# Kernel optimization log

Measured on AMD Instinct MI355X. Metric: run time of the kernel, lower is better.

## Reference

```python
import jax, jax.numpy as jnp
import numpy as np

H = 8   # n_heads
C = 2   # top-k scale factor: topk = int(C * log(L))


def setup_inputs() -> dict:
    key = jax.random.key(0)
    k1, k2, k3 = jax.random.split(key, 3)
    B, L, D = 16, 512, 4096  # L == D // H required by the original broadcasting
    Q = jax.random.normal(k1, (B, L, D), dtype=jnp.float32)
    K = jax.random.normal(k2, (B, L, D), dtype=jnp.float32)
    V = jax.random.normal(k3, (B, L, D), dtype=jnp.float32)
    return {"Q": Q, "K": K, "V": V}


def _autocorrelation(Q, K, V):
    B, L, D = Q.shape
    d = D // H
    # [B,L,D] -> [B,H,L,d]
    q = Q.reshape(B, L, H, d).transpose(0, 2, 1, 3)
    k = K.reshape(B, L, H, d).transpose(0, 2, 1, 3)
    v = V.reshape(B, L, H, d).transpose(0, 2, 1, 3)
    # FFT-based autocorrelation along the time axis (per head, per channel)
    qf = jnp.fft.fft(q, axis=2)
    kf = jnp.fft.fft(k, axis=2)
    corr = jnp.fft.ifft(qf * jnp.conj(kf), axis=2).real  # [B,H,L,d]
    topk = int(C * np.log(L))  # static: 12 for L=512
    # top-k delays per (batch, head, channel): move L to last axis
    w, idx = jax.lax.top_k(corr.transpose(0, 1, 3, 2), topk)  # [B,H,d,topk]
    w = jax.nn.softmax(w, axis=-1)
    pos = jnp.arange(L)[:, None]  # [L,1]
    out = jnp.zeros_like(v)       # [B,H,L,d]
    # small fixed loop over topk ~ O(log L) delays: gather + scale + accumulate
    for i in range(topk):
        g = jnp.minimum(idx[:, :, None, :, i] + pos, L - 1)        # [B,H,L,d]
        out = out + w[:, :, None, :, i] * jnp.take_along_axis(v, g, axis=2)
    return out.transpose(0, 2, 1, 3).reshape(B, L, D)


def reference(Q, K, V):
    return _autocorrelation(Q, K, V)
```

## Files before the change

kernel.cpp:

```cpp
#include <hip/hip_runtime.h>

#define L_LEN 512
#define D_DIM 4096
#define H_NUM 8
#define B_NUM 16
#define TOPK  12


#define LOADQK(QV, KV, QWOFF, TOFF) do {                                      \
    _Pragma("unroll")                                                         \
    for (int x = 0; x < 4; ++x) {                                             \
      const float4 v = *(const float4*)(qc + (QWOFF) + 4 * x);                \
      QV[4*x+0] = v.x; QV[4*x+1] = v.y; QV[4*x+2] = v.z; QV[4*x+3] = v.w;     \
    }                                                                         \
    _Pragma("unroll")                                                         \
    for (int x = 0; x < 4; ++x) {                                             \
      const float4 v = *(const float4*)(qc + (QWOFF) + 20 + 4 * x);           \
      QV[16+4*x+0] = v.x; QV[16+4*x+1] = v.y;                                 \
      QV[16+4*x+2] = v.z; QV[16+4*x+3] = v.w;                                 \
    }                                                                         \
    _Pragma("unroll")                                                         \
    for (int x = 0; x < 4; ++x) {                                             \
      const float4 v = *(const float4*)(kc + (TOFF) + 4 * x);                 \
      KV[4*x+0] = v.x; KV[4*x+1] = v.y; KV[4*x+2] = v.z; KV[4*x+3] = v.w;     \
    }                                                                         \
  } while (0)

#define MACBLK(QV, KV) do {                                                   \
    _Pragma("unroll")                                                         \
    for (int tt = 0; tt < 16; ++tt)                                           \
      _Pragma("unroll")                                                       \
      for (int ii = 0; ii < 16; ++ii)                                         \
        acc[ii] = fmaf(QV[ii + tt], KV[tt], acc[ii]);                         \
  } while (0)

__global__ __launch_bounds__(256, 2) void corr_topk_kernel(
    const float* __restrict__ Q, const float* __restrict__ K,
    float* __restrict__ ws_w, int* __restrict__ ws_i)
{
  __shared__ float qs[8][1312];
  __shared__ float ks[8][544];

  const int tid = threadIdx.x;
  const int bid = blockIdx.x;
  const int work = (bid & 7) * 1024 + (bid >> 3);
  const int bh   = work >> 6;
  const int cblk = work & 63;
  const int c0   = cblk * 8;

  const size_t base = (size_t)(bh >> 3) * (size_t)(L_LEN * D_DIM)
                    + (size_t)(bh & 7) * 512 + c0;

  #pragma unroll
  for (int rep = 0; rep < 4; ++rep) {
    const int idx  = rep * 256 + tid;
    const int t    = idx >> 1;
    const int half = idx & 1;
    const float4 qv = *(const float4*)(Q + base + (size_t)t * D_DIM + half * 4);
    const float4 kv = *(const float4*)(K + base + (size_t)t * D_DIM + half * 4);
    const int w  = t + ((t >> 4) << 2);
    const int cb = half * 4;
    const float qa[4] = {qv.x, qv.y, qv.z, qv.w};
    const float ka[4] = {kv.x, kv.y, kv.z, kv.w};
    #pragma unroll
    for (int j = 0; j < 4; ++j) {
      qs[cb + j][w]       = qa[j];
      qs[cb + j][w + 640] = qa[j];
      ks[cb + j][t]       = ka[j];
    }
  }
  __syncthreads();

  const int wave = tid >> 6;
  const int lane = tid & 63;
  const int ch   = wave * 2 + (lane >> 5);
  const int m    = lane & 31;

  const float* __restrict__ qc = qs[ch];
  const float* __restrict__ kc = ks[ch];

  float acc[16];
  #pragma unroll
  for (int i = 0; i < 16; ++i) acc[i] = 0.f;

  int qw = 20 * m;
  float qvA[32], kvA[16], qvB[32], kvB[16];
  LOADQK(qvA, kvA, qw, 0);
  #pragma unroll 1
  for (int t0 = 0; t0 < 512; t0 += 32) {
    LOADQK(qvB, kvB, qw + 20, t0 + 16);
    MACBLK(qvA, kvA);
    LOADQK(qvA, kvA, qw + 40, t0 + 32);
    MACBLK(qvB, kvB);
    qw += 40;
  }

  const int tau0 = m * 16;
  float bv[TOPK]; int bi[TOPK];
  #pragma unroll
  for (int s = 0; s < TOPK; ++s) {
    float lv = acc[0]; int li = 0;
    #pragma unroll
    for (int i = 1; i < 16; ++i) if (acc[i] > lv) { lv = acc[i]; li = i; }
    int gi = tau0 + li;
    #pragma unroll
    for (int off = 16; off >= 1; off >>= 1) {
      const float ov = __shfl_xor(lv, off, 32);
      const int   oi = __shfl_xor(gi, off, 32);
      if (ov > lv || (ov == lv && oi < gi)) { lv = ov; gi = oi; }
    }
    bv[s] = lv; bi[s] = gi;
    const int slot = gi - tau0;
    #pragma unroll
    for (int i = 0; i < 16; ++i) acc[i] = (slot == i) ? -3.4e38f : acc[i];
  }

  float e[TOPK]; float sum = 0.f;
  #pragma unroll
  for (int s = 0; s < TOPK; ++s) { e[s] = expf(bv[s] - bv[0]); sum += e[s]; }
  const float inv = 1.f / sum;

  if (m == 0) {
    const int g = (bh * 512 + c0 + ch) * TOPK;
    #pragma unroll
    for (int s = 0; s < TOPK; ++s) { ws_w[g + s] = e[s] * inv; ws_i[g + s] = bi[s]; }
  }
}

__global__ __launch_bounds__(512, 4) void gather_kernel(
    const float* __restrict__ V, const float* __restrict__ ws_w,
    const int* __restrict__ ws_i, float* __restrict__ out)
{
  __shared__ float vs[512][32];

  const int tid = threadIdx.x;
  const int bid = blockIdx.x;
  const int work = (bid & 7) * 256 + (bid >> 3);
  const int b  = work >> 7;
  const int dg = work & 127;
  const int d0 = dg * 32;
  const int h  = d0 >> 9;
  const int c0 = d0 & 511;

  const size_t vcol = (size_t)b * (size_t)(L_LEN * D_DIM) + d0;

  const int cl   = tid & 31;
  const int tsub = tid >> 5;

  float4 stga, stgb;
  const int e0 = tid, e1 = 512 + tid;
  const int ra0 = e0 >> 3, qa0 = (e0 & 7) * 4;
  const int rb0 = e1 >> 3, qb0 = (e1 & 7) * 4;

  stga = *(const float4*)(V + vcol + (size_t)(3 * 128 + ra0) * D_DIM + qa0);
  stgb = *(const float4*)(V + vcol + (size_t)(3 * 128 + rb0) * D_DIM + qb0);

  const int g = ((b * 8 + h) * 512 + c0 + cl) * TOPK;
  float w[TOPK]; int r0[TOPK];
  #pragma unroll
  for (int s = 0; s < TOPK; ++s) { w[s] = ws_w[g + s]; r0[s] = ws_i[g + s]; }

  const size_t ob = vcol + cl;

  #pragma unroll 1
  for (int ph = 3; ph >= 0; --ph) {
    *(float4*)(&vs[ph * 128 + ra0][qa0]) = stga;
    *(float4*)(&vs[ph * 128 + rb0][qb0]) = stgb;
    if (ph > 0) {
      stga = *(const float4*)(V + vcol + (size_t)((ph - 1) * 128 + ra0) * D_DIM + qa0);
      stgb = *(const float4*)(V + vcol + (size_t)((ph - 1) * 128 + rb0) * D_DIM + qb0);
    }
    asm volatile("s_waitcnt lgkmcnt(0)" ::: "memory");
    __builtin_amdgcn_s_barrier();
    asm volatile("" ::: "memory");

    #pragma unroll
    for (int k8 = 0; k8 < 8; ++k8) {
      const int t = ph * 128 + (k8 << 4) + tsub;
      float a = 0.f;
      #pragma unroll
      for (int s = 0; s < TOPK; ++s) {
        int r = r0[s] + t;
        r = r > (L_LEN - 1) ? (L_LEN - 1) : r;
        a = fmaf(w[s], vs[r][cl], a);
      }
      out[ob + (size_t)t * D_DIM] = a;
    }
  }
}

extern "C" void kernel_launch(void* const* d_in, const int* in_sizes, int n_in,
                              void* d_out, int out_size, void* d_ws, size_t ws_size,
                              hipStream_t stream)
{
  const float* Q = (const float*)d_in[0];
  const float* K = (const float*)d_in[1];
  const float* V = (const float*)d_in[2];
  float* out = (float*)d_out;

  float* ws_w = (float*)d_ws;
  int*   ws_i = (int*)((char*)d_ws + (size_t)B_NUM * H_NUM * 512 * TOPK * sizeof(float));

  corr_topk_kernel<<<dim3(B_NUM * H_NUM * 64), dim3(256), 0, stream>>>(Q, K, ws_w, ws_i);
  gather_kernel<<<dim3(B_NUM * H_NUM * 16), dim3(512), 0, stream>>>(V, ws_w, ws_i, out);
}
```

Baseline: 808.3 us.

## Map one channel per wave with 8 lags per lane and XOR-swizzled LDS

The correlation kernel now uses 512 threads per block. Each wave owns one channel and each lane computes 8 lags instead of 16, which cuts accumulator and register pressure and raises the occupancy target. Q is stored in LDS with an XOR swizzle in place of padding, and a rolling 32-entry register buffer replaces the double-buffered Q/K register arrays. The top-k reduction now shuffles across the full 64-lane wave. In exchange, each lane has fewer FMAs per LDS load, which lowers arithmetic intensity per LDS access.

```diff
diff --git a/kernel.cpp b/kernel.cpp
--- a/kernel.cpp
+++ b/kernel.cpp
@@ -7,112 +7,121 @@
 #define TOPK  12
 
 
-#define LOADQK(QV, KV, QWOFF, TOFF) do {                                      \
-    _Pragma("unroll")                                                         \
-    for (int x = 0; x < 4; ++x) {                                             \
-      const float4 v = *(const float4*)(qc + (QWOFF) + 4 * x);                \
-      QV[4*x+0] = v.x; QV[4*x+1] = v.y; QV[4*x+2] = v.z; QV[4*x+3] = v.w;     \
-    }                                                                         \
-    _Pragma("unroll")                                                         \
-    for (int x = 0; x < 4; ++x) {                                             \
-      const float4 v = *(const float4*)(qc + (QWOFF) + 20 + 4 * x);           \
-      QV[16+4*x+0] = v.x; QV[16+4*x+1] = v.y;                                 \
-      QV[16+4*x+2] = v.z; QV[16+4*x+3] = v.w;                                 \
-    }                                                                         \
-    _Pragma("unroll")                                                         \
-    for (int x = 0; x < 4; ++x) {                                             \
-      const float4 v = *(const float4*)(kc + (TOFF) + 4 * x);                 \
-      KV[4*x+0] = v.x; KV[4*x+1] = v.y; KV[4*x+2] = v.z; KV[4*x+3] = v.w;     \
-    }                                                                         \
+#define QADDR(W) (qc + (((((W) >> 2) ^ (((W) >> 5) & 1)) << 2) | ((W) & 3)))
+
+#define ITER(P, I) do {                                                      \
+    const int t0 = (I) * 16;                                                 \
+    const float4 r0_ = *(const float4*)QADDR(tau0 + t0 + 32);                \
+    const float4 r1_ = *(const float4*)QADDR(tau0 + t0 + 36);                \
+    const float4 r2_ = *(const float4*)QADDR(tau0 + t0 + 40);                \
+    const float4 r3_ = *(const float4*)QADDR(tau0 + t0 + 44);                \
+    const float4 ka_ = *(const float4*)(kc + t0);                            \
+    const float4 kb_ = *(const float4*)(kc + t0 + 4);                        \
+    {                                                                        \
+      const float kk[8] = {ka_.x,ka_.y,ka_.z,ka_.w, kb_.x,kb_.y,kb_.z,kb_.w};\
+      _Pragma("unroll")                                                      \
+      for (int tt = 0; tt < 8; ++tt)                                         \
+        _Pragma("unroll")                                                    \
+        for (int ii = 0; ii < 8; ++ii)                                       \
+          acc[ii] = fmaf(qb[((P) + ii + tt) & 31], kk[tt], acc[ii]);         \
+    }                                                                        \
+    const float4 kc_ = *(const float4*)(kc + t0 + 8);                        \
+    const float4 kd_ = *(const float4*)(kc + t0 + 12);                       \
+    {                                                                        \
+      const float kk[8] = {kc_.x,kc_.y,kc_.z,kc_.w, kd_.x,kd_.y,kd_.z,kd_.w};\
+      _Pragma("unroll")                                                      \
+      for (int tt = 0; tt < 8; ++tt)                                         \
+        _Pragma("unroll")                                                    \
+        for (int ii = 0; ii < 8; ++ii)                                       \
+          acc[ii] = fmaf(qb[((P) + 8 + ii + tt) & 31], kk[tt], acc[ii]);     \
+    }                                                                        \
+    qb[(P)+ 0]=r0_.x; qb[(P)+ 1]=r0_.y; qb[(P)+ 2]=r0_.z; qb[(P)+ 3]=r0_.w;  \
+    qb[(P)+ 4]=r1_.x; qb[(P)+ 5]=r1_.y; qb[(P)+ 6]=r1_.z; qb[(P)+ 7]=r1_.w;  \
+    qb[(P)+ 8]=r2_.x; qb[(P)+ 9]=r2_.y; qb[(P)+10]=r2_.z; qb[(P)+11]=r2_.w;  \
+    qb[(P)+12]=r3_.x; qb[(P)+13]=r3_.y; qb[(P)+14]=r3_.z; qb[(P)+15]=r3_.w;  \
   } while (0)
 
-#define MACBLK(QV, KV) do {                                                   \
-    _Pragma("unroll")                                                         \
-    for (int tt = 0; tt < 16; ++tt)                                           \
-      _Pragma("unroll")                                                       \
-      for (int ii = 0; ii < 16; ++ii)                                         \
-        acc[ii] = fmaf(QV[ii + tt], KV[tt], acc[ii]);                         \
-  } while (0)
-
-__global__ __launch_bounds__(256, 2) void corr_topk_kernel(
+__global__ __launch_bounds__(512, 4) void corr_topk_kernel(
     const float* __restrict__ Q, const float* __restrict__ K,
     float* __restrict__ ws_w, int* __restrict__ ws_i)
 {
-  __shared__ float qs[8][1312];
-  __shared__ float ks[8][544];
+  __shared__ float qs[8][1056];
+  __shared__ float ks[8][512];
 
   const int tid = threadIdx.x;
   const int bid = blockIdx.x;
   const int work = (bid & 7) * 1024 + (bid >> 3);
   const int bh   = work >> 6;
-  const int cblk = work & 63;
-  const int c0   = cblk * 8;
+  const int c0   = (work & 63) * 8;
 
   const size_t base = (size_t)(bh >> 3) * (size_t)(L_LEN * D_DIM)
                     + (size_t)(bh & 7) * 512 + c0;
 
   #pragma unroll
-  for (int rep = 0; rep < 4; ++rep) {
-    const int idx  = rep * 256 + tid;
+  for (int rep = 0; rep < 2; ++rep) {
+    const int idx  = rep * 512 + tid;
     const int t    = idx >> 1;
     const int half = idx & 1;
     const float4 qv = *(const float4*)(Q + base + (size_t)t * D_DIM + half * 4);
     const float4 kv = *(const float4*)(K + base + (size_t)t * D_DIM + half * 4);
-    const int w  = t + ((t >> 4) << 2);
+    const int pw = ((((t >> 2) ^ ((t >> 5) & 1)) << 2) | (t & 3));
     const int cb = half * 4;
     const float qa[4] = {qv.x, qv.y, qv.z, qv.w};
     const float ka[4] = {kv.x, kv.y, kv.z, kv.w};
     #pragma unroll
     for (int j = 0; j < 4; ++j) {
-      qs[cb + j][w]       = qa[j];
-      qs[cb + j][w + 640] = qa[j];
-      ks[cb + j][t]       = ka[j];
+      qs[cb + j][pw]       = qa[j];
+      qs[cb + j][pw + 512] = qa[j];
+      ks[cb + j][t]        = ka[j];
+    }
+    if (t < 32) {
+      #pragma unroll
+      for (int j = 0; j < 4; ++j) qs[cb + j][pw + 1024] = qa[j];
     }
   }
   __syncthreads();
 
-  const int wave = tid >> 6;
+  const int wv   = __builtin_amdgcn_readfirstlane(tid >> 6);
   const int lane = tid & 63;
-  const int ch   = wave * 2 + (lane >> 5);
-  const int m    = lane & 31;
-
-  const float* __restrict__ qc = qs[ch];
-  const float* __restrict__ kc = ks[ch];
-
-  float acc[16];
-  #pragma unroll
-  for (int i = 0; i < 16; ++i) acc[i] = 0.f;
-
-  int qw = 20 * m;
-  float qvA[32], kvA[16], qvB[32], kvB[16];
-  LOADQK(qvA, kvA, qw, 0);
+  const int tau0 = lane * 8;
+
+  const float* __restrict__ qc = qs[wv];
+  const float* __restrict__ kc = ks[wv];
+
+  float acc[8];
+  #pragma unroll
+  for (int i = 0; i < 8; ++i) acc[i] = 0.f;
+
+  float qb[32];
+  #pragma unroll
+  for (int x = 0; x < 8; ++x) {
+    const float4 v = *(const float4*)QADDR(tau0 + 4 * x);
+    qb[4*x] = v.x; qb[4*x+1] = v.y; qb[4*x+2] = v.z; qb[4*x+3] = v.w;
+  }
+
   #pragma unroll 1
-  for (int t0 = 0; t0 < 512; t0 += 32) {
-    LOADQK(qvB, kvB, qw + 20, t0 + 16);
-    MACBLK(qvA, kvA);
-    LOADQK(qvA, kvA, qw + 40, t0 + 32);
-    MACBLK(qvB, kvB);
-    qw += 40;
-  }
-
-  const int tau0 = m * 16;
+  for (int i = 0; i < 32; i += 2) {
+    ITER(0, i);
+    ITER(16, i + 1);
+  }
+
   float bv[TOPK]; int bi[TOPK];
   #pragma unroll
   for (int s = 0; s < TOPK; ++s) {
     float lv = acc[0]; int li = 0;
     #pragma unroll
-    for (int i = 1; i < 16; ++i) if (acc[i] > lv) { lv = acc[i]; li = i; }
+    for (int i = 1; i < 8; ++i) if (acc[i] > lv) { lv = acc[i]; li = i; }
     int gi = tau0 + li;
     #pragma unroll
-    for (int off = 16; off >= 1; off >>= 1) {
-      const float ov = __shfl_xor(lv, off, 32);
-      const int   oi = __shfl_xor(gi, off, 32);
+    for (int off = 32; off >= 1; off >>= 1) {
+      const float ov = __shfl_xor(lv, off, 64);
+      const int   oi = __shfl_xor(gi, off, 64);
       if (ov > lv || (ov == lv && oi < gi)) { lv = ov; gi = oi; }
     }
     bv[s] = lv; bi[s] = gi;
     const int slot = gi - tau0;
     #pragma unroll
-    for (int i = 0; i < 16; ++i) acc[i] = (slot == i) ? -3.4e38f : acc[i];
+    for (int i = 0; i < 8; ++i) acc[i] = (slot == i) ? -3.4e38f : acc[i];
   }
 
   float e[TOPK]; float sum = 0.f;
@@ -120,8 +129,8 @@
   for (int s = 0; s < TOPK; ++s) { e[s] = expf(bv[s] - bv[0]); sum += e[s]; }
   const float inv = 1.f / sum;
 
-  if (m == 0) {
-    const int g = (bh * 512 + c0 + ch) * TOPK;
+  if (lane == 0) {
+    const int g = (bh * 512 + c0 + wv) * TOPK;
     #pragma unroll
     for (int s = 0; s < TOPK; ++s) { ws_w[g + s] = e[s] * inv; ws_i[g + s] = bi[s]; }
   }
@@ -152,8 +161,8 @@
   const int ra0 = e0 >> 3, qa0 = (e0 & 7) * 4;
   const int rb0 = e1 >> 3, qb0 = (e1 & 7) * 4;
 
-  stga = *(const float4*)(V + vcol + (size_t)(3 * 128 + ra0) * D_DIM + qa0);
-  stgb = *(const float4*)(V + vcol + (size_t)(3 * 128 + rb0) * D_DIM + qb0);
+  stga = *(const float4*)(V + vcol + (size_t)(384 + ra0) * D_DIM + qa0);
+  stgb = *(const float4*)(V + vcol + (size_t)(384 + rb0) * D_DIM + qb0);
 
   const int g = ((b * 8 + h) * 512 + c0 + cl) * TOPK;
   float w[TOPK]; int r0[TOPK];
@@ -201,6 +210,6 @@
   float* ws_w = (float*)d_ws;
   int*   ws_i = (int*)((char*)d_ws + (size_t)B_NUM * H_NUM * 512 * TOPK * sizeof(float));
 
-  corr_topk_kernel<<<dim3(B_NUM * H_NUM * 64), dim3(256), 0, stream>>>(Q, K, ws_w, ws_i);
+  corr_topk_kernel<<<dim3(B_NUM * H_NUM * 64), dim3(512), 0, stream>>>(Q, K, ws_w, ws_i);
   gather_kernel<<<dim3(B_NUM * H_NUM * 16), dim3(512), 0, stream>>>(V, ws_w, ws_i, out);
 }
```

Result: slower. 866.6 us (+7.2%).
